# Optimization experiments

Hardware: AMD Instinct MI355X
Metric: run time of the kernel (lower is better)

## Reference

```python
import jax, jax.numpy as jnp
import numpy as np

EPS_BN = 1e-5
EPS_LN = 1e-5


def _gcn_conv(x, W, b, src, dst, n_nodes):
    # PyG GCNConv: h = x @ W, add self-loops, symmetric deg^{-1/2} normalization,
    # scatter-add over edges, then + bias.
    h = x @ W                                            # [N, out]
    ones = jnp.ones(src.shape[0], dtype=h.dtype)
    deg = jax.ops.segment_sum(ones, dst, num_segments=n_nodes) + 1.0  # +1 for self-loop
    dinv = jax.lax.rsqrt(deg)                            # [N]
    coef = dinv[src] * dinv[dst]                         # [E]
    msg = h[src] * coef[:, None]                         # [E, out] gather + scale
    agg = jax.ops.segment_sum(msg, dst, num_segments=n_nodes)
    agg = agg + h * (dinv * dinv)[:, None]               # self-loop contribution
    return agg + b


def _encode(x, edge_index, W1, b1, bn_gamma, bn_beta, W2, b2, ln_gamma, ln_beta, lin_W, lin_b):
    n = x.shape[0]
    src, dst = edge_index[0], edge_index[1]
    h = _gcn_conv(x, W1, b1, src, dst, n)
    # BatchNorm1d (training mode: batch statistics over nodes, biased var)
    mu = jnp.mean(h, axis=0)
    var = jnp.mean((h - mu) ** 2, axis=0)
    h = (h - mu) * jax.lax.rsqrt(var + EPS_BN) * bn_gamma + bn_beta
    h = jax.nn.relu(h)
    h = _gcn_conv(h, W2, b2, src, dst, n)
    # LayerNorm over feature dim
    mu2 = jnp.mean(h, axis=-1, keepdims=True)
    var2 = jnp.mean((h - mu2) ** 2, axis=-1, keepdims=True)
    h = (h - mu2) * jax.lax.rsqrt(var2 + EPS_LN) * ln_gamma + ln_beta
    h = jax.nn.relu(h)
    return h @ lin_W + lin_b


def setup_inputs() -> dict:
    key = jax.random.key(0)
    ks = jax.random.split(key, 16)
    N, E, EL = 100000, 800000, 200000
    C_in, C_hid, C_out = 128, 256, 128
    inp = {}
    inp["x"] = jax.random.normal(ks[0], (N, C_in), dtype=jnp.float32)
    inp["edge_index"] = jax.random.randint(ks[1], (2, E), 0, N, dtype=jnp.int64)
    inp["edge_label_index"] = jax.random.randint(ks[2], (2, EL), 0, N, dtype=jnp.int64)
    inp["cutoff"] = jnp.zeros((), dtype=jnp.float32)
    s1 = 1.0 / np.sqrt(C_in)
    s2 = 1.0 / np.sqrt(C_hid)
    s3 = 1.0 / np.sqrt(C_out)
    inp["W1"] = jax.random.uniform(ks[3], (C_in, C_hid), jnp.float32, -s1, s1)
    inp["b1"] = jnp.zeros((C_hid,), jnp.float32)
    inp["bn_gamma"] = jnp.ones((C_hid,), jnp.float32)
    inp["bn_beta"] = jnp.zeros((C_hid,), jnp.float32)
    inp["W2"] = jax.random.uniform(ks[4], (C_hid, C_out), jnp.float32, -s2, s2)
    inp["b2"] = jnp.zeros((C_out,), jnp.float32)
    inp["ln_gamma"] = jnp.ones((C_out,), jnp.float32)
    inp["ln_beta"] = jnp.zeros((C_out,), jnp.float32)
    inp["lin_W"] = jax.random.uniform(ks[5], (C_out, C_out), jnp.float32, -s3, s3)
    inp["lin_b"] = jax.random.uniform(ks[6], (C_out,), jnp.float32, -s3, s3)
    return inp


def reference(x, edge_index, edge_label_index, cutoff, W1, b1, bn_gamma, bn_beta, W2, b2, ln_gamma, ln_beta, lin_W, lin_b):
    z = _encode(x, edge_index, W1, b1, bn_gamma, bn_beta, W2, b2, ln_gamma, ln_beta, lin_W, lin_b)
    # decode: per-pair dot product + thresholding
    edge_values = jnp.sum(z[edge_label_index[0]] * z[edge_label_index[1]], axis=-1)  # [EL]
    rounded = jnp.where(edge_values < cutoff, jnp.zeros_like(edge_values), jnp.ones_like(edge_values))
    return edge_values, jax.lax.stop_gradient(rounded)
```

## Files before the change

kernel.cpp:

```cpp
#include <hip/hip_runtime.h>
#include <stdint.h>


#define C_IN  128
#define C_HID 256
#define C_OUT 128
#define SCAN_B 256

typedef __attribute__((ext_vector_type(8))) short bf16x8;
typedef __attribute__((ext_vector_type(4))) float f32x4;

__device__ __forceinline__ short f2bf(float f) {
  union { float f; uint32_t u; } v; v.f = f;
  uint32_t r = v.u + 0x7FFFu + ((v.u >> 16) & 1u);
  return (short)(r >> 16);
}
__device__ __forceinline__ uint32_t pack_bf2(float a, float b) {
  return (uint32_t)(uint16_t)f2bf(a) | ((uint32_t)(uint16_t)f2bf(b) << 16);
}
__device__ __forceinline__ float bflo(uint32_t p) {
  union { uint32_t u; float f; } v; v.u = p << 16; return v.f;
}
__device__ __forceinline__ float bfhi(uint32_t p) {
  union { uint32_t u; float f; } v; v.u = p & 0xffff0000u; return v.f;
}
__device__ __forceinline__ float bfs(short s) {
  union { uint32_t u; float f; } v; v.u = ((uint32_t)(uint16_t)s) << 16; return v.f;
}

__device__ __forceinline__ void acc8(float* a, uint4 p, float w) {
  a[0] += bflo(p.x) * w; a[1] += bfhi(p.x) * w;
  a[2] += bflo(p.y) * w; a[3] += bfhi(p.y) * w;
  a[4] += bflo(p.z) * w; a[5] += bfhi(p.z) * w;
  a[6] += bflo(p.w) * w; a[7] += bfhi(p.w) * w;
}

__device__ __forceinline__ void async_cp16(const void* g, void* l) {
  __builtin_amdgcn_global_load_lds((const __attribute__((address_space(1))) void*)g,
                                   (__attribute__((address_space(3))) void*)l, 16, 0, 0);
}


__global__ __launch_bounds__(256) void hist_kernel(const int* __restrict__ dst,
                                                   int* __restrict__ counts,
                                                   int* __restrict__ ofs, int E) {
  int e = blockIdx.x * 256 + threadIdx.x;
  if (e < E) ofs[e] = atomicAdd(&counts[dst[e]], 1);
}

__global__ __launch_bounds__(256) void dinv_kernel(const int* __restrict__ counts,
                                                   float* __restrict__ dinv, int N) {
  int n = blockIdx.x * 256 + threadIdx.x;
  if (n < N) dinv[n] = rsqrtf((float)counts[n] + 1.0f);
}


__global__ __launch_bounds__(256) void scan_part(const int* __restrict__ counts,
                                                 int* __restrict__ blockSums,
                                                 int n, int per) {
  __shared__ int ws[4];
  int b = blockIdx.x;
  int start = b * per, end = min(n, start + per);
  int s = 0;
  for (int i = start + threadIdx.x; i < end; i += 256) s += counts[i];
#pragma unroll
  for (int d = 1; d < 64; d <<= 1) s += __shfl_xor(s, d);
  if ((threadIdx.x & 63) == 0) ws[threadIdx.x >> 6] = s;
  __syncthreads();
  if (threadIdx.x == 0) blockSums[b] = ws[0] + ws[1] + ws[2] + ws[3];
}

__global__ __launch_bounds__(256) void scan_bsums(const int* __restrict__ blockSums,
                                                  int* __restrict__ blockOffs, int B) {
  __shared__ int wsum[4];
  int tid = threadIdx.x, lane = tid & 63, wid = tid >> 6;
  int v = (tid < B) ? blockSums[tid] : 0;
  int x = v;
#pragma unroll
  for (int d = 1; d < 64; d <<= 1) {
    int y = __shfl_up(x, d, 64);
    if (lane >= d) x += y;
  }
  if (lane == 63) wsum[wid] = x;
  __syncthreads();
  if (tid == 0) {
    int run = 0;
#pragma unroll
    for (int w = 0; w < 4; ++w) { int t = wsum[w]; wsum[w] = run; run += t; }
  }
  __syncthreads();
  if (tid < B) blockOffs[tid] = wsum[wid] + x - v;
}

__global__ __launch_bounds__(256) void scan_final(const int* __restrict__ counts,
                                                  const int* __restrict__ blockOffs,
                                                  int* __restrict__ row_ptr,
                                                  int n, int per) {
  __shared__ int wsum[4];
  __shared__ int sbase;
  int tid = threadIdx.x, lane = tid & 63, wid = tid >> 6;
  int b = blockIdx.x;
  int start = b * per, end = min(n + 1, start + per);
  if (tid == 0) sbase = blockOffs[b];
  __syncthreads();
  for (int chunk = start; chunk < end; chunk += 256) {
    int idx = chunk + tid;
    int v = (idx < n) ? counts[idx] : 0;
    int x = v;
#pragma unroll
    for (int d = 1; d < 64; d <<= 1) {
      int y = __shfl_up(x, d, 64);
      if (lane >= d) x += y;
    }
    if (lane == 63) wsum[wid] = x;
    __syncthreads();
    if (tid == 0) {
      int run = sbase;
#pragma unroll
      for (int w = 0; w < 4; ++w) { int t = wsum[w]; wsum[w] = run; run += t; }
      sbase = run;
    }
    __syncthreads();
    if (idx < end) row_ptr[idx] = wsum[wid] + x - v;
    __syncthreads();
  }
}

__global__ __launch_bounds__(256) void place_kernel(const int* __restrict__ src,
                                                    const int* __restrict__ dst,
                                                    const int* __restrict__ row_ptr,
                                                    const int* __restrict__ ofs,
                                                    const float* __restrict__ dinv,
                                                    int2* __restrict__ edges, int E) {
  int e = blockIdx.x * 256 + threadIdx.x;
  if (e < E) {
    int d = dst[e], s = src[e];
    int pos = row_ptr[d] + ofs[e];
    int2 ed; ed.x = s; ed.y = __float_as_int(dinv[s] * dinv[d]);
    edges[pos] = ed;
  }
}


__global__ __launch_bounds__(256) void cvt_bf16_kernel(const float* __restrict__ in,
                                                       short* __restrict__ out, int n4) {
  int i = blockIdx.x * 256 + threadIdx.x;
  if (i >= n4) return;
  float4 v = ((const float4*)in)[i];
  short4 o;
  o.x = f2bf(v.x); o.y = f2bf(v.y); o.z = f2bf(v.z); o.w = f2bf(v.w);
  ((short4*)out)[i] = o;
}

__global__ __launch_bounds__(256) void cvt_w_all(const float* __restrict__ W1,
                                                 short* __restrict__ w1t,
                                                 const float* __restrict__ W2,
                                                 short* __restrict__ w2t,
                                                 const float* __restrict__ W3,
                                                 short* __restrict__ w3t) {
  int i = blockIdx.x * 256 + threadIdx.x;
  if (i < 32768) {
    int k = i >> 8, n = i & 255;
    w1t[n * 128 + k] = f2bf(W1[i]);
  } else if (i < 65536) {
    int j = i - 32768; int k = j >> 7, n = j & 127;
    w2t[n * 256 + k] = f2bf(W2[j]);
  } else if (i < 81920) {
    int j = i - 65536; int k = j >> 7, n = j & 127;
    w3t[n * 128 + k] = f2bf(W3[j]);
  }
}


template <int MODE>
__global__ __launch_bounds__(256, 2) void bgemm_big(const short* __restrict__ A,
                                                    const short* __restrict__ BT,
                                                    const float* __restrict__ bias,
                                                    short* __restrict__ Cout,
                                                    float* __restrict__ pS,
                                                    float* __restrict__ pSS,
                                                    const float* __restrict__ bnp,
                                                    int M, int N, int K) {
  __shared__ short smem[2 * 128 * 128];
  short* As = smem;
  short* Bs = smem + 128 * 128;
  const int tid = threadIdx.x;
  const int w = tid >> 6, lane = tid & 63;
  const int wM = w >> 1, wN = w & 1;
  const int rowBase = blockIdx.y * 128;
  const int colBase = blockIdx.x * 128;
  const int l15 = lane & 15, q = lane >> 4;

  f32x4 acc[4][4];
#pragma unroll
  for (int i = 0; i < 4; ++i)
#pragma unroll
    for (int j = 0; j < 4; ++j) acc[i][j] = (f32x4){0.f, 0.f, 0.f, 0.f};

  for (int k0 = 0; k0 < K; k0 += 128) {
    if (MODE == 3) {
#pragma unroll
      for (int it = 0; it < 8; ++it) {
        int p = it * 256 + tid;
        int row = p >> 4, kcp = p & 15;
        int kc = kcp ^ (row & 15);
        int gm = rowBase + row; if (gm >= M) gm = M - 1;
        int c = k0 + kc * 8;
        bf16x8 av = *(const bf16x8*)&A[(size_t)gm * K + c];
        float4 s0 = *(const float4*)&bnp[c];
        float4 s1 = *(const float4*)&bnp[c + 4];
        float4 h0 = *(const float4*)&bnp[K + c];
        float4 h1 = *(const float4*)&bnp[K + c + 4];
        short res[8];
        res[0] = f2bf(fmaxf(bfs(av[0]) * s0.x + h0.x, 0.f));
        res[1] = f2bf(fmaxf(bfs(av[1]) * s0.y + h0.y, 0.f));
        res[2] = f2bf(fmaxf(bfs(av[2]) * s0.z + h0.z, 0.f));
        res[3] = f2bf(fmaxf(bfs(av[3]) * s0.w + h0.w, 0.f));
        res[4] = f2bf(fmaxf(bfs(av[4]) * s1.x + h1.x, 0.f));
        res[5] = f2bf(fmaxf(bfs(av[5]) * s1.y + h1.y, 0.f));
        res[6] = f2bf(fmaxf(bfs(av[6]) * s1.z + h1.z, 0.f));
        res[7] = f2bf(fmaxf(bfs(av[7]) * s1.w + h1.w, 0.f));
        bf16x8 rv;
#pragma unroll
        for (int j = 0; j < 8; ++j) rv[j] = res[j];
        *(bf16x8*)&As[p * 8] = rv;
      }
    } else {
#pragma unroll
      for (int it = 0; it < 8; ++it) {
        int p = it * 256 + tid;
        int row = p >> 4, kcp = p & 15;
        int kc = kcp ^ (row & 15);
        int gm = rowBase + row; if (gm >= M) gm = M - 1;
        async_cp16(A + (size_t)gm * K + k0 + kc * 8, &As[(it * 256 + w * 64) * 8]);
      }
    }
#pragma unroll
    for (int it = 0; it < 8; ++it) {
      int p = it * 256 + tid;
      int row = p >> 4, kcp = p & 15;
      int kc = kcp ^ (row & 15);
      async_cp16(BT + (size_t)(colBase + row) * K + k0 + kc * 8,
                 &Bs[(it * 256 + w * 64) * 8]);
    }
    __syncthreads();

#pragma unroll
    for (int ks = 0; ks < 4; ++ks) {
      bf16x8 af[4], bfr[4];
#pragma unroll
      for (int tm = 0; tm < 4; ++tm) {
        int row = wM * 64 + tm * 16 + l15;
        int kcp = (ks * 4 + q) ^ l15;
        af[tm] = *(const bf16x8*)&As[(row * 16 + kcp) * 8];
      }
#pragma unroll
      for (int tn = 0; tn < 4; ++tn) {
        int row = wN * 64 + tn * 16 + l15;
        int kcp = (ks * 4 + q) ^ l15;
        bfr[tn] = *(const bf16x8*)&Bs[(row * 16 + kcp) * 8];
      }
#pragma unroll
      for (int tm = 0; tm < 4; ++tm)
#pragma unroll
        for (int tn = 0; tn < 4; ++tn)
          acc[tm][tn] = __builtin_amdgcn_mfma_f32_16x16x32_bf16(af[tm], bfr[tn],
                                                                acc[tm][tn], 0, 0, 0);
    }
    __syncthreads();
  }

  if (MODE == 2) {
#pragma unroll
    for (int tn = 0; tn < 4; ++tn) {
      int col = colBase + wN * 64 + tn * 16 + l15;
      float bv = bias ? bias[col] : 0.0f;
      float s = 0.f, ss = 0.f;
#pragma unroll
      for (int tm = 0; tm < 4; ++tm) {
        int r0 = rowBase + wM * 64 + tm * 16 + q * 4;
#pragma unroll
        for (int r = 0; r < 4; ++r) {
          if (r0 + r < M) { float v = acc[tm][tn][r] + bv; s += v; ss += v * v; }
        }
      }
      s += __shfl_xor(s, 16); s += __shfl_xor(s, 32);
      ss += __shfl_xor(ss, 16); ss += __shfl_xor(ss, 32);
      if (q == 0) {
        int prow = blockIdx.y * 2 + wM;
        pS[(size_t)prow * C_HID + col] = s;
        pSS[(size_t)prow * C_HID + col] = ss;
      }
    }
  }

  {
    short* S = As;
#pragma unroll
    for (int tn = 0; tn < 4; ++tn) {
      int col = wN * 64 + tn * 16 + l15;
      float bv = bias ? bias[colBase + col] : 0.0f;
#pragma unroll
      for (int tm = 0; tm < 4; ++tm) {
        int r0 = wM * 64 + tm * 16 + q * 4;
#pragma unroll
        for (int r = 0; r < 4; ++r) S[(r0 + r) * 128 + col] = f2bf(acc[tm][tn][r] + bv);
      }
    }
    __syncthreads();
#pragma unroll
    for (int it = 0; it < 8; ++it) {
      int p = it * 256 + tid;
      int row = p >> 4, c = p & 15;
      int gm = rowBase + row;
      if (gm < M)
        *(uint4*)&Cout[(size_t)gm * N + colBase + c * 8] = ((const uint4*)S)[p];
    }
  }
}


__global__ __launch_bounds__(256) void bn_red1_kernel(const float* __restrict__ pS,
                                                      const float* __restrict__ pSS,
                                                      float* __restrict__ oS,
                                                      float* __restrict__ oSS, int R) {
  int c = threadIdx.x;
  int per = (R + gridDim.x - 1) / gridDim.x;
  int r0 = blockIdx.x * per, r1 = min(R, r0 + per);
  float s = 0.f, ss = 0.f;
  for (int r = r0; r < r1; ++r) {
    s += pS[(size_t)r * C_HID + c];
    ss += pSS[(size_t)r * C_HID + c];
  }
  oS[(size_t)blockIdx.x * C_HID + c] = s;
  oSS[(size_t)blockIdx.x * C_HID + c] = ss;
}

__global__ __launch_bounds__(256) void bn_red2_kernel(const float* __restrict__ oS,
                                                      const float* __restrict__ oSS,
                                                      const float* __restrict__ gamma,
                                                      const float* __restrict__ beta,
                                                      float* __restrict__ bnp,
                                                      int G, float invN) {
  int c = threadIdx.x;
  float s = 0.f, ss = 0.f;
  for (int g = 0; g < G; ++g) {
    s += oS[(size_t)g * C_HID + c];
    ss += oSS[(size_t)g * C_HID + c];
  }
  float mu = s * invN;
  float var = ss * invN - mu * mu;
  float sc = gamma[c] * rsqrtf(var + 1e-5f);
  bnp[c] = sc;
  bnp[C_HID + c] = beta[c] - mu * sc;
}


__global__ __launch_bounds__(256) void agg_x_kernel(const uint4* __restrict__ xb4,
                                                    const float* __restrict__ dinv,
                                                    const int* __restrict__ row_ptr,
                                                    const int2* __restrict__ edges,
                                                    uint4* __restrict__ out4, int N) {
  int g = (blockIdx.x * 256 + threadIdx.x) >> 4;
  int sl = threadIdx.x & 15;
  if (g >= N) return;
  int e0 = row_ptr[g], e1 = row_ptr[g + 1];
  float a[8] = {0.f, 0.f, 0.f, 0.f, 0.f, 0.f, 0.f, 0.f};
  int e = e0;
  for (; e + 4 <= e1; e += 4) {
    int2 ed0 = edges[e], ed1 = edges[e + 1], ed2 = edges[e + 2], ed3 = edges[e + 3];
    uint4 p0 = xb4[(size_t)ed0.x * 16 + sl];
    uint4 p1 = xb4[(size_t)ed1.x * 16 + sl];
    uint4 p2 = xb4[(size_t)ed2.x * 16 + sl];
    uint4 p3 = xb4[(size_t)ed3.x * 16 + sl];
    acc8(a, p0, __int_as_float(ed0.y));
    acc8(a, p1, __int_as_float(ed1.y));
    acc8(a, p2, __int_as_float(ed2.y));
    acc8(a, p3, __int_as_float(ed3.y));
  }
  for (; e < e1; ++e) {
    int2 ed = edges[e];
    uint4 p = xb4[(size_t)ed.x * 16 + sl];
    acc8(a, p, __int_as_float(ed.y));
  }
  float dn = dinv[g];
  uint4 ps = xb4[(size_t)g * 16 + sl];
  acc8(a, ps, dn * dn);
  uint4 o;
  o.x = pack_bf2(a[0], a[1]); o.y = pack_bf2(a[2], a[3]);
  o.z = pack_bf2(a[4], a[5]); o.w = pack_bf2(a[6], a[7]);
  out4[(size_t)g * 16 + sl] = o;
}

__global__ __launch_bounds__(256) void agg_ln_kernel(const uint4* __restrict__ hb4,
                                                     const float* __restrict__ dinv,
                                                     const int* __restrict__ row_ptr,
                                                     const int2* __restrict__ edges,
                                                     const float* __restrict__ bias,
                                                     const float* __restrict__ gamma,
                                                     const float* __restrict__ beta,
                                                     uint4* __restrict__ zb4, int N) {
  int g = (blockIdx.x * 256 + threadIdx.x) >> 4;
  int sl = threadIdx.x & 15;
  if (g >= N) return;
  int e0 = row_ptr[g], e1 = row_ptr[g + 1];
  float a[8] = {0.f, 0.f, 0.f, 0.f, 0.f, 0.f, 0.f, 0.f};
  int e = e0;
  for (; e + 4 <= e1; e += 4) {
    int2 ed0 = edges[e], ed1 = edges[e + 1], ed2 = edges[e + 2], ed3 = edges[e + 3];
    uint4 p0 = hb4[(size_t)ed0.x * 16 + sl];
    uint4 p1 = hb4[(size_t)ed1.x * 16 + sl];
    uint4 p2 = hb4[(size_t)ed2.x * 16 + sl];
    uint4 p3 = hb4[(size_t)ed3.x * 16 + sl];
    acc8(a, p0, __int_as_float(ed0.y));
    acc8(a, p1, __int_as_float(ed1.y));
    acc8(a, p2, __int_as_float(ed2.y));
    acc8(a, p3, __int_as_float(ed3.y));
  }
  for (; e < e1; ++e) {
    int2 ed = edges[e];
    uint4 p = hb4[(size_t)ed.x * 16 + sl];
    acc8(a, p, __int_as_float(ed.y));
  }
  float dn = dinv[g];
  uint4 ps = hb4[(size_t)g * 16 + sl];
  acc8(a, ps, dn * dn);

  int c = sl * 8;
  float4 bv0 = *(const float4*)&bias[c];
  float4 bv1 = *(const float4*)&bias[c + 4];
  a[0] += bv0.x; a[1] += bv0.y; a[2] += bv0.z; a[3] += bv0.w;
  a[4] += bv1.x; a[5] += bv1.y; a[6] += bv1.z; a[7] += bv1.w;

  float s = 0.f, ss = 0.f;
#pragma unroll
  for (int j = 0; j < 8; ++j) { s += a[j]; ss += a[j] * a[j]; }
#pragma unroll
  for (int d = 1; d < 16; d <<= 1) {
    s += __shfl_xor(s, d);
    ss += __shfl_xor(ss, d);
  }
  float mu = s * (1.0f / C_OUT);
  float var = ss * (1.0f / C_OUT) - mu * mu;
  float rs = rsqrtf(var + 1e-5f);
  float4 g0 = *(const float4*)&gamma[c];
  float4 g1 = *(const float4*)&gamma[c + 4];
  float4 t0 = *(const float4*)&beta[c];
  float4 t1 = *(const float4*)&beta[c + 4];
  float o[8];
  o[0] = fmaxf((a[0] - mu) * rs * g0.x + t0.x, 0.0f);
  o[1] = fmaxf((a[1] - mu) * rs * g0.y + t0.y, 0.0f);
  o[2] = fmaxf((a[2] - mu) * rs * g0.z + t0.z, 0.0f);
  o[3] = fmaxf((a[3] - mu) * rs * g0.w + t0.w, 0.0f);
  o[4] = fmaxf((a[4] - mu) * rs * g1.x + t1.x, 0.0f);
  o[5] = fmaxf((a[5] - mu) * rs * g1.y + t1.y, 0.0f);
  o[6] = fmaxf((a[6] - mu) * rs * g1.z + t1.z, 0.0f);
  o[7] = fmaxf((a[7] - mu) * rs * g1.w + t1.w, 0.0f);
  uint4 ov;
  ov.x = pack_bf2(o[0], o[1]); ov.y = pack_bf2(o[2], o[3]);
  ov.z = pack_bf2(o[4], o[5]); ov.w = pack_bf2(o[6], o[7]);
  zb4[(size_t)g * 16 + sl] = ov;
}


__global__ __launch_bounds__(256) void decode_kernel(const uint4* __restrict__ zb4,
                                                     const int* __restrict__ eli,
                                                     const float* __restrict__ cutoff,
                                                     float* __restrict__ out, int EL) {
  int g = (blockIdx.x * 256 + threadIdx.x) >> 4;
  int sl = threadIdx.x & 15;
  if (g >= EL) return;
  int a = eli[g];
  int b = eli[EL + g];
  uint4 va = zb4[(size_t)a * 16 + sl];
  uint4 vb = zb4[(size_t)b * 16 + sl];
  float s = bflo(va.x) * bflo(vb.x) + bfhi(va.x) * bfhi(vb.x)
          + bflo(va.y) * bflo(vb.y) + bfhi(va.y) * bfhi(vb.y)
          + bflo(va.z) * bflo(vb.z) + bfhi(va.z) * bfhi(vb.z)
          + bflo(va.w) * bflo(vb.w) + bfhi(va.w) * bfhi(vb.w);
#pragma unroll
  for (int d = 1; d < 16; d <<= 1) s += __shfl_xor(s, d);
  if (sl == 0) {
    out[g] = s;
    out[EL + g] = (s < cutoff[0]) ? 0.0f : 1.0f;
  }
}


extern "C" void kernel_launch(void* const* d_in, const int* in_sizes, int n_in,
                              void* d_out, int out_size, void* d_ws, size_t ws_size,
                              hipStream_t stream) {
  const float* x        = (const float*)d_in[0];
  const int*   eidx     = (const int*)d_in[1];
  const int*   eli      = (const int*)d_in[2];
  const float* cutoff   = (const float*)d_in[3];
  const float* W1       = (const float*)d_in[4];
  const float* b1       = (const float*)d_in[5];
  const float* bn_gamma = (const float*)d_in[6];
  const float* bn_beta  = (const float*)d_in[7];
  const float* W2       = (const float*)d_in[8];
  const float* b2       = (const float*)d_in[9];
  const float* ln_gamma = (const float*)d_in[10];
  const float* ln_beta  = (const float*)d_in[11];
  const float* lin_W    = (const float*)d_in[12];
  const float* lin_b    = (const float*)d_in[13];
  float* out = (float*)d_out;

  const int N  = in_sizes[0] / C_IN;
  const int E  = in_sizes[1] / 2;
  const int EL = in_sizes[2] / 2;

  const int* src = eidx;
  const int* dst = eidx + E;

  const int MB = (N + 127) / 128;
  const int R  = 2 * MB;

  char* p = (char*)d_ws;
  short* regionA = (short*)p;  p += (size_t)N * 256 * 2;
  short* regionB = (short*)p;  p += (size_t)N * 256 * 2;
  short* h2_bf   = (short*)p;  p += (size_t)N * 128 * 2;
  float* dinv    = (float*)p;  p += (size_t)N * 4;
  int* counts    = (int*)p;    p += (size_t)N * 4;
  int* row_ptr   = (int*)p;    p += (size_t)(N + 4) * 4;
  int* ofs       = (int*)p;    p += (size_t)E * 4;
  int2* edges    = (int2*)p;   p += (size_t)E * 8;
  float* pS      = (float*)p;  p += (size_t)R * C_HID * 4;
  float* pSS     = (float*)p;  p += (size_t)R * C_HID * 4;
  float* oS      = (float*)p;  p += 32 * C_HID * 4;
  float* oSS     = (float*)p;  p += 32 * C_HID * 4;
  float* bnp     = (float*)p;  p += 2 * C_HID * 4;
  int* blockSums = (int*)p;    p += SCAN_B * 4;
  int* blockOffs = (int*)p;    p += SCAN_B * 4;
  short* w1t     = (short*)p;  p += (size_t)C_HID * C_IN * 2;
  short* w2t     = (short*)p;  p += (size_t)C_OUT * C_HID * 2;
  short* w3t     = (short*)p;  p += (size_t)C_OUT * C_OUT * 2;

  short* x_bf   = regionA;
  short* xa_bf  = regionA + (size_t)N * 128;
  short* h1_bf  = regionB;
  short* z_bf   = regionB;
  short* zf_bf  = regionA;

  hipMemsetAsync(counts, 0, (size_t)N * 4, stream);

  int eb = (E + 255) / 256;
  int nb = (N + 255) / 256;

  hist_kernel<<<eb, 256, 0, stream>>>(dst, counts, ofs, E);
  dinv_kernel<<<nb, 256, 0, stream>>>(counts, dinv, N);

  int per = (N + 1 + SCAN_B - 1) / SCAN_B;
  scan_part<<<SCAN_B, 256, 0, stream>>>(counts, blockSums, N, per);
  scan_bsums<<<1, 256, 0, stream>>>(blockSums, blockOffs, SCAN_B);
  scan_final<<<SCAN_B, 256, 0, stream>>>(counts, blockOffs, row_ptr, N, per);

  place_kernel<<<eb, 256, 0, stream>>>(src, dst, row_ptr, ofs, dinv, edges, E);

  cvt_w_all<<<320, 256, 0, stream>>>(W1, w1t, W2, w2t, lin_W, w3t);

  int xn4 = N * C_IN / 4;
  cvt_bf16_kernel<<<(xn4 + 255) / 256, 256, 0, stream>>>(x, x_bf, xn4);

  int gb = ((size_t)N * 16 + 255) / 256;
  agg_x_kernel<<<gb, 256, 0, stream>>>((const uint4*)x_bf, dinv, row_ptr, edges,
                                       (uint4*)xa_bf, N);

  dim3 g1(C_HID / 128, MB);
  bgemm_big<2><<<g1, 256, 0, stream>>>(xa_bf, w1t, b1, h1_bf, pS, pSS, nullptr,
                                       N, C_HID, C_IN);

  bn_red1_kernel<<<32, 256, 0, stream>>>(pS, pSS, oS, oSS, R);
  bn_red2_kernel<<<1, 256, 0, stream>>>(oS, oSS, bn_gamma, bn_beta, bnp, 32,
                                        1.0f / (float)N);

  dim3 g2(C_OUT / 128, MB);
  bgemm_big<3><<<g2, 256, 0, stream>>>(h1_bf, w2t, nullptr, h2_bf, nullptr, nullptr,
                                       bnp, N, C_OUT, C_HID);

  agg_ln_kernel<<<gb, 256, 0, stream>>>((const uint4*)h2_bf, dinv, row_ptr, edges,
                                        b2, ln_gamma, ln_beta, (uint4*)z_bf, N);

  dim3 g3(C_OUT / 128, MB);
  bgemm_big<1><<<g3, 256, 0, stream>>>(z_bf, w3t, lin_b, zf_bf, nullptr, nullptr,
                                       nullptr, N, C_OUT, C_OUT);

  int db = ((size_t)EL * 16 + 255) / 256;
  decode_kernel<<<db, 256, 0, stream>>>((const uint4*)zf_bf, eli, cutoff, out, EL);
}
```

Measured before the change: 369.4 us.

## Fuse second aggregation+LayerNorm into final GEMM and merge small setup kernels

```diff
diff --git a/kernel.cpp b/kernel.cpp
--- a/kernel.cpp
+++ b/kernel.cpp
@@ -48,21 +48,19 @@
   if (e < E) ofs[e] = atomicAdd(&counts[dst[e]], 1);
 }
 
-__global__ __launch_bounds__(256) void dinv_kernel(const int* __restrict__ counts,
-                                                   float* __restrict__ dinv, int N) {
-  int n = blockIdx.x * 256 + threadIdx.x;
-  if (n < N) dinv[n] = rsqrtf((float)counts[n] + 1.0f);
-}
-
-
 __global__ __launch_bounds__(256) void scan_part(const int* __restrict__ counts,
                                                  int* __restrict__ blockSums,
+                                                 float* __restrict__ dinv,
                                                  int n, int per) {
   __shared__ int ws[4];
   int b = blockIdx.x;
   int start = b * per, end = min(n, start + per);
   int s = 0;
-  for (int i = start + threadIdx.x; i < end; i += 256) s += counts[i];
+  for (int i = start + threadIdx.x; i < end; i += 256) {
+    int c = counts[i];
+    s += c;
+    dinv[i] = rsqrtf((float)c + 1.0f);
+  }
 #pragma unroll
   for (int d = 1; d < 64; d <<= 1) s += __shfl_xor(s, d);
   if ((threadIdx.x & 63) == 0) ws[threadIdx.x >> 6] = s;
@@ -70,39 +68,24 @@
   if (threadIdx.x == 0) blockSums[b] = ws[0] + ws[1] + ws[2] + ws[3];
 }
 
-__global__ __launch_bounds__(256) void scan_bsums(const int* __restrict__ blockSums,
-                                                  int* __restrict__ blockOffs, int B) {
-  __shared__ int wsum[4];
-  int tid = threadIdx.x, lane = tid & 63, wid = tid >> 6;
-  int v = (tid < B) ? blockSums[tid] : 0;
-  int x = v;
-#pragma unroll
-  for (int d = 1; d < 64; d <<= 1) {
-    int y = __shfl_up(x, d, 64);
-    if (lane >= d) x += y;
-  }
-  if (lane == 63) wsum[wid] = x;
-  __syncthreads();
-  if (tid == 0) {
-    int run = 0;
-#pragma unroll
-    for (int w = 0; w < 4; ++w) { int t = wsum[w]; wsum[w] = run; run += t; }
-  }
-  __syncthreads();
-  if (tid < B) blockOffs[tid] = wsum[wid] + x - v;
-}
-
 __global__ __launch_bounds__(256) void scan_final(const int* __restrict__ counts,
-                                                  const int* __restrict__ blockOffs,
+                                                  const int* __restrict__ blockSums,
                                                   int* __restrict__ row_ptr,
                                                   int n, int per) {
   __shared__ int wsum[4];
   __shared__ int sbase;
   int tid = threadIdx.x, lane = tid & 63, wid = tid >> 6;
   int b = blockIdx.x;
+  {
+    int v = (tid < b) ? blockSums[tid] : 0;
+#pragma unroll
+    for (int d = 1; d < 64; d <<= 1) v += __shfl_xor(v, d);
+    if (lane == 0) wsum[wid] = v;
+    __syncthreads();
+    if (tid == 0) sbase = wsum[0] + wsum[1] + wsum[2] + wsum[3];
+    __syncthreads();
+  }
   int start = b * per, end = min(n + 1, start + per);
-  if (tid == 0) sbase = blockOffs[b];
-  __syncthreads();
   for (int chunk = start; chunk < end; chunk += 256) {
     int idx = chunk + tid;
     int v = (idx < n) ? counts[idx] : 0;
@@ -142,32 +125,32 @@
 }
 
 
-__global__ __launch_bounds__(256) void cvt_bf16_kernel(const float* __restrict__ in,
-                                                       short* __restrict__ out, int n4) {
+__global__ __launch_bounds__(256) void cvt_all(const float* __restrict__ x,
+                                               short* __restrict__ x_bf, int n4,
+                                               const float* __restrict__ W1,
+                                               short* __restrict__ w1t,
+                                               const float* __restrict__ W2,
+                                               short* __restrict__ w2t,
+                                               const float* __restrict__ W3,
+                                               short* __restrict__ w3t) {
   int i = blockIdx.x * 256 + threadIdx.x;
-  if (i >= n4) return;
-  float4 v = ((const float4*)in)[i];
-  short4 o;
-  o.x = f2bf(v.x); o.y = f2bf(v.y); o.z = f2bf(v.z); o.w = f2bf(v.w);
-  ((short4*)out)[i] = o;
-}
-
-__global__ __launch_bounds__(256) void cvt_w_all(const float* __restrict__ W1,
-                                                 short* __restrict__ w1t,
-                                                 const float* __restrict__ W2,
-                                                 short* __restrict__ w2t,
-                                                 const float* __restrict__ W3,
-                                                 short* __restrict__ w3t) {
-  int i = blockIdx.x * 256 + threadIdx.x;
-  if (i < 32768) {
-    int k = i >> 8, n = i & 255;
-    w1t[n * 128 + k] = f2bf(W1[i]);
-  } else if (i < 65536) {
-    int j = i - 32768; int k = j >> 7, n = j & 127;
-    w2t[n * 256 + k] = f2bf(W2[j]);
-  } else if (i < 81920) {
-    int j = i - 65536; int k = j >> 7, n = j & 127;
-    w3t[n * 128 + k] = f2bf(W3[j]);
+  if (i < n4) {
+    float4 v = ((const float4*)x)[i];
+    short4 o;
+    o.x = f2bf(v.x); o.y = f2bf(v.y); o.z = f2bf(v.z); o.w = f2bf(v.w);
+    ((short4*)x_bf)[i] = o;
+    return;
+  }
+  int j = i - n4;
+  if (j < 32768) {
+    int k = j >> 8, n = j & 255;
+    w1t[n * 128 + k] = f2bf(W1[j]);
+  } else if (j < 65536) {
+    int jj = j - 32768; int k = jj >> 7, n = jj & 127;
+    w2t[n * 256 + k] = f2bf(W2[jj]);
+  } else if (j < 81920) {
+    int jj = j - 65536; int k = jj >> 7, n = jj & 127;
+    w3t[n * 128 + k] = f2bf(W3[jj]);
   }
 }
 
@@ -320,6 +303,146 @@
 }
 
 
+__global__ __launch_bounds__(256, 2) void fused_ln_gemm3(
+    const uint4* __restrict__ hb4, const float* __restrict__ dinv,
+    const int* __restrict__ row_ptr, const int2* __restrict__ edges,
+    const float* __restrict__ b2, const float* __restrict__ gamma,
+    const float* __restrict__ beta, const short* __restrict__ BT,
+    const float* __restrict__ bias, short* __restrict__ Cout, int M) {
+  __shared__ short As[128 * 128];
+  __shared__ short Bs[128 * 128];
+  const int tid = threadIdx.x;
+  const int w = tid >> 6, lane = tid & 63;
+  const int wM = w >> 1, wN = w & 1;
+  const int rowBase = blockIdx.x * 128;
+  const int l15 = lane & 15, q = lane >> 4;
+  const int g16 = tid >> 4, sl = tid & 15;
+
+#pragma unroll
+  for (int it = 0; it < 8; ++it) {
+    int p = it * 256 + tid;
+    int row = p >> 4, kcp = p & 15;
+    int kc = kcp ^ (row & 15);
+    async_cp16(BT + (size_t)row * 128 + kc * 8, &Bs[(it * 256 + w * 64) * 8]);
+  }
+
+  int c = sl * 8;
+  float4 bv0 = *(const float4*)&b2[c];
+  float4 bv1 = *(const float4*)&b2[c + 4];
+  float4 g0 = *(const float4*)&gamma[c];
+  float4 g1 = *(const float4*)&gamma[c + 4];
+  float4 t0 = *(const float4*)&beta[c];
+  float4 t1 = *(const float4*)&beta[c + 4];
+#pragma unroll
+  for (int r = 0; r < 8; ++r) {
+    int rowLocal = g16 * 8 + r;
+    int gm = rowBase + rowLocal; if (gm >= M) gm = M - 1;
+    int e0 = row_ptr[gm], e1 = row_ptr[gm + 1];
+    float a[8] = {0.f, 0.f, 0.f, 0.f, 0.f, 0.f, 0.f, 0.f};
+    int e = e0;
+    for (; e + 4 <= e1; e += 4) {
+      int2 ed0 = edges[e], ed1 = edges[e + 1], ed2 = edges[e + 2], ed3 = edges[e + 3];
+      uint4 p0 = hb4[(size_t)ed0.x * 16 + sl];
+      uint4 p1 = hb4[(size_t)ed1.x * 16 + sl];
+      uint4 p2 = hb4[(size_t)ed2.x * 16 + sl];
+      uint4 p3 = hb4[(size_t)ed3.x * 16 + sl];
+      acc8(a, p0, __int_as_float(ed0.y));
+      acc8(a, p1, __int_as_float(ed1.y));
+      acc8(a, p2, __int_as_float(ed2.y));
+      acc8(a, p3, __int_as_float(ed3.y));
+    }
+    for (; e < e1; ++e) {
+      int2 ed = edges[e];
+      uint4 p = hb4[(size_t)ed.x * 16 + sl];
+      acc8(a, p, __int_as_float(ed.y));
+    }
+    float dn = dinv[gm];
+    uint4 ps = hb4[(size_t)gm * 16 + sl];
+    acc8(a, ps, dn * dn);
+    a[0] += bv0.x; a[1] += bv0.y; a[2] += bv0.z; a[3] += bv0.w;
+    a[4] += bv1.x; a[5] += bv1.y; a[6] += bv1.z; a[7] += bv1.w;
+
+    float s = 0.f, ss = 0.f;
+#pragma unroll
+    for (int j = 0; j < 8; ++j) { s += a[j]; ss += a[j] * a[j]; }
+#pragma unroll
+    for (int d = 1; d < 16; d <<= 1) {
+      s += __shfl_xor(s, d);
+      ss += __shfl_xor(ss, d);
+    }
+    float mu = s * (1.0f / C_OUT);
+    float var = ss * (1.0f / C_OUT) - mu * mu;
+    float rs = rsqrtf(var + 1e-5f);
+    bf16x8 rv;
+    rv[0] = f2bf(fmaxf((a[0] - mu) * rs * g0.x + t0.x, 0.f));
+    rv[1] = f2bf(fmaxf((a[1] - mu) * rs * g0.y + t0.y, 0.f));
+    rv[2] = f2bf(fmaxf((a[2] - mu) * rs * g0.z + t0.z, 0.f));
+    rv[3] = f2bf(fmaxf((a[3] - mu) * rs * g0.w + t0.w, 0.f));
+    rv[4] = f2bf(fmaxf((a[4] - mu) * rs * g1.x + t1.x, 0.f));
+    rv[5] = f2bf(fmaxf((a[5] - mu) * rs * g1.y + t1.y, 0.f));
+    rv[6] = f2bf(fmaxf((a[6] - mu) * rs * g1.z + t1.z, 0.f));
+    rv[7] = f2bf(fmaxf((a[7] - mu) * rs * g1.w + t1.w, 0.f));
+    int kcp = sl ^ (rowLocal & 15);
+    *(bf16x8*)&As[(rowLocal * 16 + kcp) * 8] = rv;
+  }
+  __syncthreads();
+
+  f32x4 acc[4][4];
+#pragma unroll
+  for (int i = 0; i < 4; ++i)
+#pragma unroll
+    for (int j = 0; j < 4; ++j) acc[i][j] = (f32x4){0.f, 0.f, 0.f, 0.f};
+
+#pragma unroll
+  for (int ks = 0; ks < 4; ++ks) {
+    bf16x8 af[4], bfr[4];
+#pragma unroll
+    for (int tm = 0; tm < 4; ++tm) {
+      int row = wM * 64 + tm * 16 + l15;
+      int kcp = (ks * 4 + q) ^ l15;
+      af[tm] = *(const bf16x8*)&As[(row * 16 + kcp) * 8];
+    }
+#pragma unroll
+    for (int tn = 0; tn < 4; ++tn) {
+      int row = wN * 64 + tn * 16 + l15;
+      int kcp = (ks * 4 + q) ^ l15;
+      bfr[tn] = *(const bf16x8*)&Bs[(row * 16 + kcp) * 8];
+    }
+#pragma unroll
+    for (int tm = 0; tm < 4; ++tm)
+#pragma unroll
+      for (int tn = 0; tn < 4; ++tn)
+        acc[tm][tn] = __builtin_amdgcn_mfma_f32_16x16x32_bf16(af[tm], bfr[tn],
+                                                              acc[tm][tn], 0, 0, 0);
+  }
+  __syncthreads();
+
+  {
+    short* S = As;
+#pragma unroll
+    for (int tn = 0; tn < 4; ++tn) {
+      int col = wN * 64 + tn * 16 + l15;
+      float bv = bias[col];
+#pragma unroll
+      for (int tm = 0; tm < 4; ++tm) {
+        int r0 = wM * 64 + tm * 16 + q * 4;
+#pragma unroll
+        for (int r = 0; r < 4; ++r) S[(r0 + r) * 128 + col] = f2bf(acc[tm][tn][r] + bv);
+      }
+    }
+    __syncthreads();
+#pragma unroll
+    for (int it = 0; it < 8; ++it) {
+      int p = it * 256 + tid;
+      int row = p >> 4, cc = p & 15;
+      int gm = rowBase + row;
+      if (gm < M)
+        *(uint4*)&Cout[(size_t)gm * 128 + cc * 8] = ((const uint4*)S)[p];
+    }
+  }
+}
+
+
 __global__ __launch_bounds__(256) void bn_red1_kernel(const float* __restrict__ pS,
                                                       const float* __restrict__ pSS,
                                                       float* __restrict__ oS,
@@ -392,76 +515,6 @@
   out4[(size_t)g * 16 + sl] = o;
 }
 
-__global__ __launch_bounds__(256) void agg_ln_kernel(const uint4* __restrict__ hb4,
-                                                     const float* __restrict__ dinv,
-                                                     const int* __restrict__ row_ptr,
-                                                     const int2* __restrict__ edges,
-                                                     const float* __restrict__ bias,
-                                                     const float* __restrict__ gamma,
-                                                     const float* __restrict__ beta,
-                                                     uint4* __restrict__ zb4, int N) {
-  int g = (blockIdx.x * 256 + threadIdx.x) >> 4;
-  int sl = threadIdx.x & 15;
-  if (g >= N) return;
-  int e0 = row_ptr[g], e1 = row_ptr[g + 1];
-  float a[8] = {0.f, 0.f, 0.f, 0.f, 0.f, 0.f, 0.f, 0.f};
-  int e = e0;
-  for (; e + 4 <= e1; e += 4) {
-    int2 ed0 = edges[e], ed1 = edges[e + 1], ed2 = edges[e + 2], ed3 = edges[e + 3];
-    uint4 p0 = hb4[(size_t)ed0.x * 16 + sl];
-    uint4 p1 = hb4[(size_t)ed1.x * 16 + sl];
-    uint4 p2 = hb4[(size_t)ed2.x * 16 + sl];
-    uint4 p3 = hb4[(size_t)ed3.x * 16 + sl];
-    acc8(a, p0, __int_as_float(ed0.y));
-    acc8(a, p1, __int_as_float(ed1.y));
-    acc8(a, p2, __int_as_float(ed2.y));
-    acc8(a, p3, __int_as_float(ed3.y));
-  }
-  for (; e < e1; ++e) {
-    int2 ed = edges[e];
-    uint4 p = hb4[(size_t)ed.x * 16 + sl];
-    acc8(a, p, __int_as_float(ed.y));
-  }
-  float dn = dinv[g];
-  uint4 ps = hb4[(size_t)g * 16 + sl];
-  acc8(a, ps, dn * dn);
-
-  int c = sl * 8;
-  float4 bv0 = *(const float4*)&bias[c];
-  float4 bv1 = *(const float4*)&bias[c + 4];
-  a[0] += bv0.x; a[1] += bv0.y; a[2] += bv0.z; a[3] += bv0.w;
-  a[4] += bv1.x; a[5] += bv1.y; a[6] += bv1.z; a[7] += bv1.w;
-
-  float s = 0.f, ss = 0.f;
-#pragma unroll
-  for (int j = 0; j < 8; ++j) { s += a[j]; ss += a[j] * a[j]; }
-#pragma unroll
-  for (int d = 1; d < 16; d <<= 1) {
-    s += __shfl_xor(s, d);
-    ss += __shfl_xor(ss, d);
-  }
-  float mu = s * (1.0f / C_OUT);
-  float var = ss * (1.0f / C_OUT) - mu * mu;
-  float rs = rsqrtf(var + 1e-5f);
-  float4 g0 = *(const float4*)&gamma[c];
-  float4 g1 = *(const float4*)&gamma[c + 4];
-  float4 t0 = *(const float4*)&beta[c];
-  float4 t1 = *(const float4*)&beta[c + 4];
-  float o[8];
-  o[0] = fmaxf((a[0] - mu) * rs * g0.x + t0.x, 0.0f);
-  o[1] = fmaxf((a[1] - mu) * rs * g0.y + t0.y, 0.0f);
-  o[2] = fmaxf((a[2] - mu) * rs * g0.z + t0.z, 0.0f);
-  o[3] = fmaxf((a[3] - mu) * rs * g0.w + t0.w, 0.0f);
-  o[4] = fmaxf((a[4] - mu) * rs * g1.x + t1.x, 0.0f);
-  o[5] = fmaxf((a[5] - mu) * rs * g1.y + t1.y, 0.0f);
-  o[6] = fmaxf((a[6] - mu) * rs * g1.z + t1.z, 0.0f);
-  o[7] = fmaxf((a[7] - mu) * rs * g1.w + t1.w, 0.0f);
-  uint4 ov;
-  ov.x = pack_bf2(o[0], o[1]); ov.y = pack_bf2(o[2], o[3]);
-  ov.z = pack_bf2(o[4], o[5]); ov.w = pack_bf2(o[6], o[7]);
-  zb4[(size_t)g * 16 + sl] = ov;
-}
-
 
 __global__ __launch_bounds__(256) void decode_kernel(const uint4* __restrict__ zb4,
                                                      const int* __restrict__ eli,
@@ -531,7 +584,6 @@
   float* oSS     = (float*)p;  p += 32 * C_HID * 4;
   float* bnp     = (float*)p;  p += 2 * C_HID * 4;
   int* blockSums = (int*)p;    p += SCAN_B * 4;
-  int* blockOffs = (int*)p;    p += SCAN_B * 4;
   short* w1t     = (short*)p;  p += (size_t)C_HID * C_IN * 2;
   short* w2t     = (short*)p;  p += (size_t)C_OUT * C_HID * 2;
   short* w3t     = (short*)p;  p += (size_t)C_OUT * C_OUT * 2;
@@ -539,28 +591,23 @@
   short* x_bf   = regionA;
   short* xa_bf  = regionA + (size_t)N * 128;
   short* h1_bf  = regionB;
-  short* z_bf   = regionB;
   short* zf_bf  = regionA;
 
   hipMemsetAsync(counts, 0, (size_t)N * 4, stream);
 
   int eb = (E + 255) / 256;
-  int nb = (N + 255) / 256;
 
   hist_kernel<<<eb, 256, 0, stream>>>(dst, counts, ofs, E);
-  dinv_kernel<<<nb, 256, 0, stream>>>(counts, dinv, N);
 
   int per = (N + 1 + SCAN_B - 1) / SCAN_B;
-  scan_part<<<SCAN_B, 256, 0, stream>>>(counts, blockSums, N, per);
-  scan_bsums<<<1, 256, 0, stream>>>(blockSums, blockOffs, SCAN_B);
-  scan_final<<<SCAN_B, 256, 0, stream>>>(counts, blockOffs, row_ptr, N, per);
+  scan_part<<<SCAN_B, 256, 0, stream>>>(counts, blockSums, dinv, N, per);
+  scan_final<<<SCAN_B, 256, 0, stream>>>(counts, blockSums, row_ptr, N, per);
 
   place_kernel<<<eb, 256, 0, stream>>>(src, dst, row_ptr, ofs, dinv, edges, E);
 
-  cvt_w_all<<<320, 256, 0, stream>>>(W1, w1t, W2, w2t, lin_W, w3t);
-
   int xn4 = N * C_IN / 4;
-  cvt_bf16_kernel<<<(xn4 + 255) / 256, 256, 0, stream>>>(x, x_bf, xn4);
+  cvt_all<<<(xn4 + 81920 + 255) / 256, 256, 0, stream>>>(x, x_bf, xn4, W1, w1t,
+                                                         W2, w2t, lin_W, w3t);
 
   int gb = ((size_t)N * 16 + 255) / 256;
   agg_x_kernel<<<gb, 256, 0, stream>>>((const uint4*)x_bf, dinv, row_ptr, edges,
@@ -578,12 +625,9 @@
   bgemm_big<3><<<g2, 256, 0, stream>>>(h1_bf, w2t, nullptr, h2_bf, nullptr, nullptr,
                                        bnp, N, C_OUT, C_HID);
 
-  agg_ln_kernel<<<gb, 256, 0, stream>>>((const uint4*)h2_bf, dinv, row_ptr, edges,
-                                        b2, ln_gamma, ln_beta, (uint4*)z_bf, N);
-
-  dim3 g3(C_OUT / 128, MB);
-  bgemm_big<1><<<g3, 256, 0, stream>>>(z_bf, w3t, lin_b, zf_bf, nullptr, nullptr,
-                                       nullptr, N, C_OUT, C_OUT);
+  fused_ln_gemm3<<<MB, 256, 0, stream>>>((const uint4*)h2_bf, dinv, row_ptr, edges,
+                                         b2, ln_gamma, ln_beta, w3t, lin_b,
+                                         zf_bf, N);
 
   int db = ((size_t)EL * 16 + 255) / 256;
   decode_kernel<<<db, 256, 0, stream>>>((const uint4*)zf_bf, eli, cutoff, out, EL);
```

New measurement: 385.4 us. 4.3% more time.
